# Optimization experiments

Hardware: AMD Instinct MI355X
Metric: run time of the kernel (lower is better)

## Reference

```python
import jax, jax.numpy as jnp
import numpy as np
from jax import lax

EPS_LN = 1e-5
EPS_BN = 1e-5

def layernorm(x, g, b):
    m = x.mean(-1, keepdims=True)
    v = x.var(-1, keepdims=True)
    return (x - m) / jnp.sqrt(v + EPS_LN) * g + b

def conv(x, w, b):
    y = lax.conv_general_dilated(x, w, (1, 1), 'SAME', dimension_numbers=('NCHW', 'OIHW', 'NCHW'))
    return y + b[None, :, None, None]

def bnorm(x, g, b, m, v):
    # BatchNorm2d in eval mode (running stats)
    return (x - m[None, :, None, None]) / jnp.sqrt(v[None, :, None, None] + EPS_BN) * g[None, :, None, None] + b[None, :, None, None]

def maxpool2(x):
    return lax.reduce_window(x, -jnp.inf, lax.max, (1, 1, 2, 2), (1, 1, 2, 2), 'VALID')

def l2norm_rows(x):
    n = jnp.linalg.norm(x, axis=1, keepdims=True)
    return x / jnp.maximum(n, 1e-12)

def fastslow(x, sw, sb, fw, fb, lng, lnb, lr, decay):
    # one hebbian fast-weight update step (torch does this in no_grad on x.detach())
    xs = lax.stop_gradient(x)
    fw = fw * decay
    fb = fb * decay
    slow_out = xs @ sw.T + sb
    xn = l2norm_rows(xs)
    son = l2norm_rows(slow_out)
    hebb = son.T @ xn / xs.shape[0]          # [out,in] outer-product update
    fw = fw + lr * hebb
    wn = jnp.linalg.norm(fw, axis=1, keepdims=True)
    fw = jnp.where(wn > 0.25, fw * (0.25 / (wn + 1e-8)), fw)
    fb = jnp.clip(fb + lr * son.mean(0), -0.2, 0.2)
    fw = lax.stop_gradient(fw)
    fb = lax.stop_gradient(fb)
    out = x @ (sw + fw).T + (sb + fb)
    return layernorm(out, lng, lnb)

def forward(x, c1_w, c1_b, bn1_g, bn1_b, bn1_m, bn1_v,
            c2_w, c2_b, bn2_g, bn2_b, bn2_m, bn2_v,
            c3_w, c3_b, bn3_g, bn3_b, bn3_m, bn3_v,
            core_w, core_b, core_lng, core_lnb,
            fp_sw, fp_sb, fp_fw, fp_fb, fp_lng, fp_lnb,
            sp_sw, sp_sb, sp_fw, sp_fb, sp_lng, sp_lnb,
            int_w, int_b, int_lng, int_lnb, mem,
            cn_w1, cn_b1, cn_lng, cn_lnb, cn_w2, cn_b2,
            pr_w, pr_b, pr_lng, pr_lnb, cl_w, cl_b):
    # encoder (dropout layers are identity in eval)
    h = jax.nn.relu(bnorm(conv(x, c1_w, c1_b), bn1_g, bn1_b, bn1_m, bn1_v)); h = maxpool2(h)
    h = jax.nn.relu(bnorm(conv(h, c2_w, c2_b), bn2_g, bn2_b, bn2_m, bn2_v)); h = maxpool2(h)
    h = jax.nn.relu(bnorm(conv(h, c3_w, c3_b), bn3_g, bn3_b, bn3_m, bn3_v))
    h = h.mean((2, 3))  # AdaptiveAvgPool2d((1,1)) + Flatten -> [B,256]
    # core
    hc = jax.nn.relu(layernorm(h @ core_w.T + core_b, core_lng, core_lnb))
    # dual system: memory EMA (no_grad), fast/slow hebbian paths, integrator
    mem_new = lax.stop_gradient(0.9 * mem + 0.1 * hc.mean(0, keepdims=True))
    fast_out = fastslow(hc, fp_sw, fp_sb, fp_fw, fp_fb, fp_lng, fp_lnb, 0.015, 0.95)
    slow_out = fastslow(hc + 0.3 * mem_new, sp_sw, sp_sb, sp_fw, sp_fb, sp_lng, sp_lnb, 0.005, 0.97)
    comb = jnp.concatenate([fast_out, slow_out], axis=1)
    hd = layernorm(comb @ int_w.T + int_b, int_lng, int_lnb)
    hd = hd + hc  # residual
    # consciousness: phi from eigen-entropy of feature covariance (no_grad)
    a = lax.stop_gradient(hd)
    am = a.mean(0, keepdims=True)
    ast = jnp.std(a, axis=0, keepdims=True, ddof=1) + 1e-6
    an = (a - am) / ast
    n = a.shape[0]
    cov = an.T @ an / (n - 1) + 1e-4 * jnp.eye(a.shape[1], dtype=a.dtype)
    eigs = jnp.clip(jnp.linalg.eigvalsh(cov), 0.0, None)
    en = eigs / (eigs.sum() + 1e-8)
    entropy = -(en * jnp.log(en + 1e-8)).sum()
    phi = entropy / jnp.log(jnp.asarray(float(a.shape[1]), a.dtype))
    phi_eff = jnp.clip(0.3 * phi, 0.0, 1.0)  # running_phi starts at 0: 0.7*0 + 0.3*phi
    net = jax.nn.relu(layernorm(hd @ cn_w1.T + cn_b1, cn_lng, cn_lnb)) @ cn_w2.T + cn_b2
    strength = jax.nn.sigmoid((phi_eff - 0.1) * 5.0)
    coef = jnp.where(phi_eff > 0.1, strength, 0.1)
    hcon = hd + coef * net
    # projection + classifier
    hp = jax.nn.relu(layernorm(hcon @ pr_w.T + pr_b, pr_lng, pr_lnb))
    return hp @ cl_w.T + cl_b

def setup_inputs() -> dict:
    key = jax.random.key(0)
    ks = iter(jax.random.split(key, 64))
    def nrm(shape, s=0.05):
        return jax.random.normal(next(ks), shape, jnp.float32) * s
    B, D = 512, 256
    d = {}
    d['x'] = jax.random.normal(next(ks), (B, 3, 32, 32), jnp.float32)
    for i, (co, ci) in enumerate([(64, 3), (128, 64), (256, 128)], 1):
        d[f'c{i}_w'] = nrm((co, ci, 3, 3))
        d[f'c{i}_b'] = jnp.zeros((co,), jnp.float32)
        d[f'bn{i}_g'] = jnp.ones((co,), jnp.float32)
        d[f'bn{i}_b'] = jnp.zeros((co,), jnp.float32)
        d[f'bn{i}_m'] = jnp.zeros((co,), jnp.float32)
        d[f'bn{i}_v'] = jnp.ones((co,), jnp.float32)
    d['core_w'] = nrm((D, D)); d['core_b'] = jnp.zeros((D,), jnp.float32)
    d['core_lng'] = jnp.ones((D,), jnp.float32); d['core_lnb'] = jnp.zeros((D,), jnp.float32)
    for p in ['fp', 'sp']:
        d[f'{p}_sw'] = nrm((D, D)); d[f'{p}_sb'] = jnp.zeros((D,), jnp.float32)
        d[f'{p}_fw'] = nrm((D, D), 0.01); d[f'{p}_fb'] = jnp.zeros((D,), jnp.float32)
        d[f'{p}_lng'] = jnp.ones((D,), jnp.float32); d[f'{p}_lnb'] = jnp.zeros((D,), jnp.float32)
    d['int_w'] = nrm((D, 2 * D)); d['int_b'] = jnp.zeros((D,), jnp.float32)
    d['int_lng'] = jnp.ones((D,), jnp.float32); d['int_lnb'] = jnp.zeros((D,), jnp.float32)
    d['mem'] = jnp.zeros((1, D), jnp.float32)
    d['cn_w1'] = nrm((D, D)); d['cn_b1'] = jnp.zeros((D,), jnp.float32)
    d['cn_lng'] = jnp.ones((D,), jnp.float32); d['cn_lnb'] = jnp.zeros((D,), jnp.float32)
    d['cn_w2'] = nrm((D, D)); d['cn_b2'] = jnp.zeros((D,), jnp.float32)
    d['pr_w'] = nrm((128, D)); d['pr_b'] = jnp.zeros((128,), jnp.float32)
    d['pr_lng'] = jnp.ones((128,), jnp.float32); d['pr_lnb'] = jnp.zeros((128,), jnp.float32)
    d['cl_w'] = nrm((10, 128)); d['cl_b'] = jnp.zeros((10,), jnp.float32)
    return d

def reference(x, c1_w, c1_b, bn1_g, bn1_b, bn1_m, bn1_v,
              c2_w, c2_b, bn2_g, bn2_b, bn2_m, bn2_v,
              c3_w, c3_b, bn3_g, bn3_b, bn3_m, bn3_v,
              core_w, core_b, core_lng, core_lnb,
              fp_sw, fp_sb, fp_fw, fp_fb, fp_lng, fp_lnb,
              sp_sw, sp_sb, sp_fw, sp_fb, sp_lng, sp_lnb,
              int_w, int_b, int_lng, int_lnb, mem,
              cn_w1, cn_b1, cn_lng, cn_lnb, cn_w2, cn_b2,
              pr_w, pr_b, pr_lng, pr_lnb, cl_w, cl_b):
    return forward(x, c1_w, c1_b, bn1_g, bn1_b, bn1_m, bn1_v,
                   c2_w, c2_b, bn2_g, bn2_b, bn2_m, bn2_v,
                   c3_w, c3_b, bn3_g, bn3_b, bn3_m, bn3_v,
                   core_w, core_b, core_lng, core_lnb,
                   fp_sw, fp_sb, fp_fw, fp_fb, fp_lng, fp_lnb,
                   sp_sw, sp_sb, sp_fw, sp_fb, sp_lng, sp_lnb,
                   int_w, int_b, int_lng, int_lnb, mem,
                   cn_w1, cn_b1, cn_lng, cn_lnb, cn_w2, cn_b2,
                   pr_w, pr_b, pr_lng, pr_lnb, cl_w, cl_b)
```

## Files before the change

### kernel.cpp

```cpp
#include <hip/hip_runtime.h>
#include <hip/hip_bf16.h>

template<int NT>
__device__ __forceinline__ float block_sum(float v, float* red, int t) {
  red[t] = v; __syncthreads();
#pragma unroll
  for (int s = NT/2; s > 0; s >>= 1) {
    if (t < s) red[t] += red[t+s];
    __syncthreads();
  }
  float r = red[0];
  __syncthreads();
  return r;
}

__device__ __forceinline__ float block_sum4(float val, float* red4, int t) {
#pragma unroll
  for (int mk = 1; mk < 64; mk <<= 1) val += __shfl_xor(val, mk, 64);
  if ((t & 63) == 0) red4[t >> 6] = val;
  __syncthreads();
  float r = red4[0] + red4[1] + red4[2] + red4[3];
  __syncthreads();
  return r;
}

template<int DIN>
__device__ __forceinline__ float dot_f32_row(const float* __restrict__ wr, const float* __restrict__ xs) {
  float acc = 0.f;
  const float4* wp = reinterpret_cast<const float4*>(wr);
#pragma unroll 4
  for (int i = 0; i < DIN/4; ++i) {
    float4 w4 = wp[i];
    acc += w4.x*xs[i*4] + w4.y*xs[i*4+1] + w4.z*xs[i*4+2] + w4.w*xs[i*4+3];
  }
  return acc;
}

__global__ __launch_bounds__(256) void k_conv1(const float* __restrict__ x, const float* __restrict__ w1,
    const float* __restrict__ cb, const float* __restrict__ g, const float* __restrict__ bb,
    const float* __restrict__ m, const float* __restrict__ v, float* __restrict__ p1)
{
  __shared__ float xs[3][34][34];
  __shared__ float ws1[64*27];
  __shared__ float A1[64], B1[64];
  int b = blockIdx.x, t = threadIdx.x;
  float* xsf = &xs[0][0][0];
  for (int i = t; i < 3*34*34; i += 256) xsf[i] = 0.f;
  for (int i = t; i < 64*27; i += 256) ws1[i] = w1[i];
  if (t < 64) {
    float sc = g[t] * rsqrtf(v[t] + 1e-5f);
    A1[t] = sc;
    B1[t] = (cb[t] - m[t])*sc + bb[t];
  }
  __syncthreads();
  for (int i = t; i < 3*1024; i += 256) {
    int ci = i >> 10, rem = i & 1023, y = rem >> 5, xx = rem & 31;
    xs[ci][y+1][xx+1] = x[((size_t)b*3 + ci)*1024 + rem];
  }
  __syncthreads();
  int py = t >> 4, px = t & 15;
  int y0 = py*2, x0 = px*2;
  for (int co = 0; co < 64; ++co) {
    float a00=0.f,a01=0.f,a10=0.f,a11=0.f;
#pragma unroll
    for (int ci = 0; ci < 3; ++ci) {
      const float* xb = &xs[ci][y0][x0];
      float r0a=xb[0],r0b=xb[1],r0c=xb[2],r0d=xb[3];
      float r1a=xb[34],r1b=xb[35],r1c=xb[36],r1d=xb[37];
      float r2a=xb[68],r2b=xb[69],r2c=xb[70],r2d=xb[71];
      float r3a=xb[102],r3b=xb[103],r3c=xb[104],r3d=xb[105];
      const float* wp = &ws1[co*27 + ci*9];
      float ww0=wp[0],ww1=wp[1],ww2=wp[2],ww3=wp[3],ww4=wp[4],ww5=wp[5],ww6=wp[6],ww7=wp[7],ww8=wp[8];
      a00 += ww0*r0a+ww1*r0b+ww2*r0c + ww3*r1a+ww4*r1b+ww5*r1c + ww6*r2a+ww7*r2b+ww8*r2c;
      a01 += ww0*r0b+ww1*r0c+ww2*r0d + ww3*r1b+ww4*r1c+ww5*r1d + ww6*r2b+ww7*r2c+ww8*r2d;
      a10 += ww0*r1a+ww1*r1b+ww2*r1c + ww3*r2a+ww4*r2b+ww5*r2c + ww6*r3a+ww7*r3b+ww8*r3c;
      a11 += ww0*r1b+ww1*r1c+ww2*r1d + ww3*r2b+ww4*r2c+ww5*r2d + ww6*r3b+ww7*r3c+ww8*r3d;
    }
    float sc = A1[co], sh = B1[co];
    float vmax = fmaxf(fmaxf(a00*sc+sh, a01*sc+sh), fmaxf(a10*sc+sh, a11*sc+sh));
    vmax = fmaxf(vmax, 0.f);
    p1[(((size_t)b*64 + co)*16 + py)*16 + px] = vmax;
  }
}

__global__ __launch_bounds__(256) void k_conv2(const float* __restrict__ p1, const float* __restrict__ w2,
    const float* __restrict__ cb, const float* __restrict__ g, const float* __restrict__ bb,
    const float* __restrict__ m, const float* __restrict__ v, float* __restrict__ p2)
{
  __shared__ float xs[64][18][18];
  __shared__ float wchT[576*5];
  __shared__ float A2[128], B2[128];
  int b = blockIdx.x, t = threadIdx.x;
  float* xsf = &xs[0][0][0];
  for (int i = t; i < 64*18*18; i += 256) xsf[i] = 0.f;
  if (t < 128) {
    float sc = g[t] * rsqrtf(v[t] + 1e-5f);
    A2[t] = sc;
    B2[t] = (cb[t] - m[t])*sc + bb[t];
  }
  __syncthreads();
  for (int i = t; i < 64*256; i += 256) {
    int ci = i >> 8, rem = i & 255, y = rem >> 4, xx = rem & 15;
    xs[ci][y+1][xx+1] = p1[((size_t)b*64 + ci)*256 + rem];
  }
  int lane = t & 3, pos = t >> 2;
  int py = pos >> 3, px = pos & 7;
  int y0 = py*2, x0 = px*2;
  for (int it = 0; it < 32; ++it) {
    __syncthreads();
    for (int i = t; i < 2304; i += 256) {
      int rem = i % 576, co = i / 576;
      wchT[rem*5 + co] = w2[(size_t)it*2304 + i];
    }
    __syncthreads();
    float a00=0.f,a01=0.f,a10=0.f,a11=0.f;
    for (int ci = 0; ci < 64; ++ci) {
      const float* xb = &xs[ci][y0][x0];
      float r0a=xb[0],r0b=xb[1],r0c=xb[2],r0d=xb[3];
      float r1a=xb[18],r1b=xb[19],r1c=xb[20],r1d=xb[21];
      float r2a=xb[36],r2b=xb[37],r2c=xb[38],r2d=xb[39];
      float r3a=xb[54],r3b=xb[55],r3c=xb[56],r3d=xb[57];
      const float* wp = &wchT[(ci*9)*5 + lane];
      float ww0=wp[0],ww1=wp[5],ww2=wp[10],ww3=wp[15],ww4=wp[20],ww5=wp[25],ww6=wp[30],ww7=wp[35],ww8=wp[40];
      a00 += ww0*r0a+ww1*r0b+ww2*r0c + ww3*r1a+ww4*r1b+ww5*r1c + ww6*r2a+ww7*r2b+ww8*r2c;
      a01 += ww0*r0b+ww1*r0c+ww2*r0d + ww3*r1b+ww4*r1c+ww5*r1d + ww6*r2b+ww7*r2c+ww8*r2d;
      a10 += ww0*r1a+ww1*r1b+ww2*r1c + ww3*r2a+ww4*r2b+ww5*r2c + ww6*r3a+ww7*r3b+ww8*r3c;
      a11 += ww0*r1b+ww1*r1c+ww2*r1d + ww3*r2b+ww4*r2c+ww5*r2d + ww6*r3b+ww7*r3c+ww8*r3d;
    }
    int co = it*4 + lane;
    float sc = A2[co], sh = B2[co];
    float vmax = fmaxf(fmaxf(a00*sc+sh, a01*sc+sh), fmaxf(a10*sc+sh, a11*sc+sh));
    vmax = fmaxf(vmax, 0.f);
    p2[(((size_t)b*128 + co)*8 + py)*8 + px] = vmax;
  }
}

__global__ __launch_bounds__(256) void k_conv3(const float* __restrict__ p2, const float* __restrict__ w3,
    const float* __restrict__ cb, const float* __restrict__ g, const float* __restrict__ bb,
    const float* __restrict__ m, const float* __restrict__ v, float* __restrict__ h)
{
  __shared__ float xs[128][10][10];
  __shared__ float wchT[1152*17];
  __shared__ float A3[256], B3[256];
  __shared__ float red2[256];
  int b = blockIdx.x, t = threadIdx.x;
  float* xsf = &xs[0][0][0];
  for (int i = t; i < 128*100; i += 256) xsf[i] = 0.f;
  {
    float sc = g[t] * rsqrtf(v[t] + 1e-5f);
    A3[t] = sc;
    B3[t] = (cb[t] - m[t])*sc + bb[t];
  }
  __syncthreads();
  for (int i = t; i < 128*64; i += 256) {
    int ci = i >> 6, rem = i & 63, y = rem >> 3, xx = rem & 7;
    xs[ci][y+1][xx+1] = p2[((size_t)b*128 + ci)*64 + rem];
  }
  int lane = t & 15, cluster = t >> 4;
  int cy = cluster >> 2, cx = cluster & 3;
  int y0 = cy*2, x0 = cx*2;
  for (int it = 0; it < 16; ++it) {
    __syncthreads();
    for (int i = t; i < 18432; i += 256) {
      int rem = i % 1152, co = i / 1152;
      wchT[rem*17 + co] = w3[(size_t)it*18432 + i];
    }
    __syncthreads();
    float a00=0.f,a01=0.f,a10=0.f,a11=0.f;
    for (int ci = 0; ci < 128; ++ci) {
      const float* xb = &xs[ci][y0][x0];
      float r0a=xb[0],r0b=xb[1],r0c=xb[2],r0d=xb[3];
      float r1a=xb[10],r1b=xb[11],r1c=xb[12],r1d=xb[13];
      float r2a=xb[20],r2b=xb[21],r2c=xb[22],r2d=xb[23];
      float r3a=xb[30],r3b=xb[31],r3c=xb[32],r3d=xb[33];
      const float* wp = &wchT[(ci*9)*17 + lane];
      float ww0=wp[0],ww1=wp[17],ww2=wp[34],ww3=wp[51],ww4=wp[68],ww5=wp[85],ww6=wp[102],ww7=wp[119],ww8=wp[136];
      a00 += ww0*r0a+ww1*r0b+ww2*r0c + ww3*r1a+ww4*r1b+ww5*r1c + ww6*r2a+ww7*r2b+ww8*r2c;
      a01 += ww0*r0b+ww1*r0c+ww2*r0d + ww3*r1b+ww4*r1c+ww5*r1d + ww6*r2b+ww7*r2c+ww8*r2d;
      a10 += ww0*r1a+ww1*r1b+ww2*r1c + ww3*r2a+ww4*r2b+ww5*r2c + ww6*r3a+ww7*r3b+ww8*r3c;
      a11 += ww0*r1b+ww1*r1c+ww2*r1d + ww3*r2b+ww4*r2c+ww5*r2d + ww6*r3b+ww7*r3c+ww8*r3d;
    }
    int co = it*16 + lane;
    float sc = A3[co], sh = B3[co];
    float local = fmaxf(a00*sc+sh,0.f)+fmaxf(a01*sc+sh,0.f)+fmaxf(a10*sc+sh,0.f)+fmaxf(a11*sc+sh,0.f);
    red2[cluster*16 + lane] = local;
    __syncthreads();
    if (t < 16) {
      float s2 = 0.f;
      for (int c2 = 0; c2 < 16; ++c2) s2 += red2[c2*16 + t];
      h[(size_t)b*256 + it*16 + t] = s2 * (1.f/64.f);
    }
  }
}

template<int DIN, int DOUT, bool RELU, bool RESID>
__global__ __launch_bounds__(DOUT) void k_lin_ln(
    const float* __restrict__ in, const float* __restrict__ W, const float* __restrict__ bias,
    const float* __restrict__ g, const float* __restrict__ be,
    const float* __restrict__ resid, float* __restrict__ out, int ostride, int ooff)
{
  __shared__ float xs[DIN];
  __shared__ float red[DOUT];
  int b = blockIdx.x, t = threadIdx.x;
  for (int i = t; i < DIN; i += DOUT) xs[i] = in[(size_t)b*DIN + i];
  __syncthreads();
  float acc = dot_f32_row<DIN>(W + (size_t)t*DIN, xs) + bias[t];
  float mean = block_sum<DOUT>(acc, red, t) * (1.f/DOUT);
  float dv = acc - mean;
  float var = block_sum<DOUT>(dv*dv, red, t) * (1.f/DOUT);
  float y = dv * rsqrtf(var + 1e-5f) * g[t] + be[t];
  if (RELU) y = fmaxf(y, 0.f);
  if (RESID) y += resid[(size_t)b*DOUT + t];
  out[(size_t)b*ostride + ooff + t] = y;
}

__global__ __launch_bounds__(256) void k_lin_rownorm(const float* __restrict__ in, const float* __restrict__ sw,
    const float* __restrict__ sb, float* __restrict__ sout, float* __restrict__ xninv, float* __restrict__ sninv)
{
  int b = blockIdx.x, t = threadIdx.x;
  __shared__ float xs[256];
  __shared__ float red[256];
  xs[t] = in[(size_t)b*256 + t];
  __syncthreads();
  float acc = dot_f32_row<256>(sw + (size_t)t*256, xs) + sb[t];
  sout[(size_t)b*256 + t] = acc;
  float xn2 = block_sum<256>(xs[t]*xs[t], red, t);
  float sn2 = block_sum<256>(acc*acc, red, t);
  if (t == 0) {
    xninv[b] = 1.f / fmaxf(sqrtf(xn2), 1e-12f);
    sninv[b] = 1.f / fmaxf(sqrtf(sn2), 1e-12f);
  }
}

__global__ __launch_bounds__(256) void k_hebb(const float* __restrict__ x, const float* __restrict__ s,
    const float* __restrict__ xninv, const float* __restrict__ sninv,
    const float* __restrict__ sw, const float* __restrict__ fw,
    const float* __restrict__ sb, const float* __restrict__ fb,
    float lr, float decay, float* __restrict__ weff, float* __restrict__ beff)
{
  int o = blockIdx.x, t = threadIdx.x;
  __shared__ float c[512];
  __shared__ float sonb[512];
  __shared__ float red[256];
  for (int b = t; b < 512; b += 256) {
    float son = s[(size_t)b*256 + o] * sninv[b];
    sonb[b] = son;
    c[b] = son * xninv[b];
  }
  __syncthreads();
  float acc = 0.f;
  for (int b = 0; b < 512; ++b) acc += c[b] * x[(size_t)b*256 + t];
  float hebb = acc * (1.f/512.f);
  float fwn = fw[(size_t)o*256 + t] * decay + lr * hebb;
  float wn2 = block_sum<256>(fwn*fwn, red, t);
  float wn = sqrtf(wn2);
  float scale = (wn > 0.25f) ? 0.25f/(wn + 1e-8f) : 1.f;
  weff[(size_t)o*256 + t] = sw[(size_t)o*256 + t] + fwn*scale;
  float sm = block_sum<256>(sonb[t] + sonb[t+256], red, t) * (1.f/512.f);
  if (t == 0) {
    float fbe = fb[o] * decay + lr * sm;
    fbe = fminf(fmaxf(fbe, -0.2f), 0.2f);
    beff[o] = sb[o] + fbe;
  }
}

__global__ __launch_bounds__(256) void k_mem(const float* __restrict__ hc, const float* __restrict__ mem,
                                             float* __restrict__ memnew)
{
  int t = threadIdx.x;
  float s = 0.f;
  for (int b = 0; b < 512; ++b) s += hc[(size_t)b*256 + t];
  memnew[t] = 0.9f*mem[t] + 0.1f*(s * (1.f/512.f));
}

__global__ __launch_bounds__(256) void k_x2(const float* __restrict__ hc, const float* __restrict__ memnew,
                                            float* __restrict__ x2)
{
  int i = blockIdx.x*256 + threadIdx.x;
  x2[i] = hc[i] + 0.3f*memnew[i & 255];
}

__global__ __launch_bounds__(256) void k_colstats(const float* __restrict__ hd, float* __restrict__ am,
                                                  float* __restrict__ ainv)
{
  int t = threadIdx.x;
  float s1 = 0.f;
  for (int b = 0; b < 512; ++b) s1 += hd[(size_t)b*256 + t];
  float mean = s1 * (1.f/512.f);
  float s2 = 0.f;
  for (int b = 0; b < 512; ++b) { float dv = hd[(size_t)b*256 + t] - mean; s2 += dv*dv; }
  am[t] = mean;
  ainv[t] = 1.f/(sqrtf(s2 * (1.f/511.f)) + 1e-6f);
}

__global__ __launch_bounds__(256) void k_cov(const float* __restrict__ hd, const float* __restrict__ am,
    const float* __restrict__ ainv, float* __restrict__ cov)
{
  int i = blockIdx.x, t = threadIdx.x;
  __shared__ float ci[512];
  float ami = am[i], aii = ainv[i];
  for (int b = t; b < 512; b += 256) ci[b] = (hd[(size_t)b*256 + i] - ami)*aii;
  __syncthreads();
  float amj = am[t], aij = ainv[t];
  float acc = 0.f;
  for (int b = 0; b < 512; ++b) acc += ci[b] * (hd[(size_t)b*256 + t] - amj);
  float cval = acc * aij * (1.f/511.f) + ((i == t) ? 1e-4f : 0.f);
  cov[(size_t)i*256 + t] = cval;
}

__global__ __launch_bounds__(256) void k_tridiag(const float* __restrict__ A, float* __restrict__ d, float* __restrict__ e)
{
  const int n = 256;
  __shared__ float tri[32896];
  __shared__ float v[256], q[256];
  __shared__ float red4[4];
  __shared__ float sH, salpha;
  int t = threadIdx.x;

  for (int i = t; i < 32896; i += 256) {
    int r = (int)((sqrtf(8.f*(float)i + 1.f) - 1.f) * 0.5f);
    while ((r+1)*(r+2)/2 <= i) ++r;
    while (r*(r+1)/2 > i) --r;
    int c = i - r*(r+1)/2;
    tri[i] = A[(size_t)r*n + c];
  }
  __syncthreads();

  for (int k = 0; k < n-2; ++k) {
    int m = n-1-k;
    int base = k+1;
    int R = base + t;
    int offA = (R*(R+1))/2 + base;
    float xi = (t < m) ? tri[offA - 1] : 0.f;
    float sigma = block_sum4(xi*xi, red4, t);
    if (t == 0) {
      float x0 = tri[(base*(base+1))/2 + k];
      float alpha = (x0 >= 0.f) ? -sqrtf(sigma) : sqrtf(sigma);
      salpha = alpha;
      sH = sigma - x0*alpha;
      e[k] = alpha;
    }
    __syncthreads();
    float H = sH;
    if (H <= 1e-32f) { __syncthreads(); continue; }
    if (t < m) v[t] = (t == 0) ? (xi - salpha) : xi;
    __syncthreads();

    float pt = 0.f;
    if (t < m) {
      float a0 = 0.f, a1 = 0.f, a2 = 0.f, a3 = 0.f;
      int j = 0;
      for (; j + 4 <= t+1; j += 4) {
        a0 += tri[offA + j]     * v[j];
        a1 += tri[offA + j + 1] * v[j+1];
        a2 += tri[offA + j + 2] * v[j+2];
        a3 += tri[offA + j + 3] * v[j+3];
      }
      for (; j <= t; ++j) a0 += tri[offA + j] * v[j];
      int Rj = R + 1;
      int off = (Rj*(Rj+1))/2 + R;
      for (j = t+1; j + 4 <= m; j += 4) {
        int o0 = off;
        int o1 = o0 + (base + j + 1);
        int o2 = o1 + (base + j + 2);
        int o3 = o2 + (base + j + 3);
        a0 += tri[o0] * v[j];
        a1 += tri[o1] * v[j+1];
        a2 += tri[o2] * v[j+2];
        a3 += tri[o3] * v[j+3];
        off = o3 + (base + j + 4);
      }
      for (; j < m; ++j) {
        a0 += tri[off] * v[j];
        off += (base + j + 1);
      }
      pt = (a0 + a1 + a2 + a3) / H;
    }
    float Kv = block_sum4((t < m) ? v[t]*pt : 0.f, red4, t) / (2.f*H);
    if (t < m) q[t] = pt - Kv*v[t];
    __syncthreads();

    if (t < m) {
      float vt = v[t], qt = q[t];
      int c = 0;
      for (; c + 4 <= t+1; c += 4) {
        float u0 = tri[offA + c]     - (vt*q[c]   + qt*v[c]);
        float u1 = tri[offA + c + 1] - (vt*q[c+1] + qt*v[c+1]);
        float u2 = tri[offA + c + 2] - (vt*q[c+2] + qt*v[c+2]);
        float u3 = tri[offA + c + 3] - (vt*q[c+3] + qt*v[c+3]);
        tri[offA + c]     = u0;
        tri[offA + c + 1] = u1;
        tri[offA + c + 2] = u2;
        tri[offA + c + 3] = u3;
      }
      for (; c <= t; ++c) tri[offA + c] -= vt*q[c] + qt*v[c];
    }
    __syncthreads();
  }
  if (t == 0) {
    e[n-2] = tri[((n-1)*n)/2 + (n-2)];
    e[n-1] = 0.f;
  }
  d[t] = tri[(t*(t+1))/2 + t];
}

__global__ __launch_bounds__(256) void k_eig_coef(const float* __restrict__ dg, const float* __restrict__ eg,
                                                  float* __restrict__ coefout)
{
  const int n = 256;
  int t = threadIdx.x;
  __shared__ float sd[256], se2[256], sea[256], red[256];
  sd[t] = dg[t];
  float ev = (t < n-1) ? eg[t] : 0.f;
  se2[t] = ev*ev;
  sea[t] = fabsf(ev);
  __syncthreads();
  float r = ((t > 0) ? sea[t-1] : 0.f) + sea[t];
  red[t] = sd[t] - r; __syncthreads();
  for (int s = 128; s > 0; s >>= 1) { if (t < s) red[t] = fminf(red[t], red[t+s]); __syncthreads(); }
  float glo = red[0] - 1e-3f; __syncthreads();
  red[t] = sd[t] + r; __syncthreads();
  for (int s = 128; s > 0; s >>= 1) { if (t < s) red[t] = fmaxf(red[t], red[t+s]); __syncthreads(); }
  float ghi = red[0] + 1e-3f; __syncthreads();

  float lo = glo, hi = ghi;
  for (int it = 0; it < 40; ++it) {
    float mid = 0.5f*(lo + hi);
    int cnt = 0;
    float qq = sd[0] - mid;
    cnt += (qq < 0.f);
    for (int i = 1; i < n; ++i) {
      float denom = qq;
      if (fabsf(denom) < 1e-20f) denom = (denom < 0.f) ? -1e-20f : 1e-20f;
      qq = sd[i] - mid - se2[i-1]/denom;
      cnt += (qq < 0.f);
    }
    if (cnt <= t) lo = mid; else hi = mid;
  }
  float lam = fmaxf(0.5f*(lo + hi), 0.f);
  float tot = block_sum<256>(lam, red, t) + 1e-8f;
  float en = lam / tot;
  float contrib = -en * logf(en + 1e-8f);
  float ent = block_sum<256>(contrib, red, t);
  if (t == 0) {
    float phi = ent / logf(256.f);
    float phi_eff = fminf(fmaxf(0.3f*phi, 0.f), 1.f);
    float strength = 1.f/(1.f + expf(-(phi_eff - 0.1f)*5.f));
    coefout[0] = (phi_eff > 0.1f) ? strength : 0.1f;
  }
}

__global__ __launch_bounds__(256) void k_cn2(const float* __restrict__ t1, const float* __restrict__ W,
    const float* __restrict__ bias, const float* __restrict__ hd, const float* __restrict__ coefp,
    float* __restrict__ hcon)
{
  __shared__ float xs[256];
  int b = blockIdx.x, t = threadIdx.x;
  xs[t] = t1[(size_t)b*256 + t];
  __syncthreads();
  float acc = dot_f32_row<256>(W + (size_t)t*256, xs) + bias[t];
  hcon[(size_t)b*256 + t] = hd[(size_t)b*256 + t] + coefp[0]*acc;
}

__global__ __launch_bounds__(64) void k_cls(const float* __restrict__ hp, const float* __restrict__ W,
    const float* __restrict__ bias, float* __restrict__ out)
{
  int b = blockIdx.x, t = threadIdx.x;
  __shared__ float xs[128];
  if (t < 64) { xs[t] = hp[(size_t)b*128 + t]; xs[t+64] = hp[(size_t)b*128 + t + 64]; }
  __syncthreads();
  if (t < 10) {
    float acc = bias[t];
    const float* wr = W + (size_t)t*128;
    for (int i = 0; i < 128; ++i) acc += wr[i]*xs[i];
    out[(size_t)b*10 + t] = acc;
  }
}

extern "C" void kernel_launch(void* const* d_in, const int* in_sizes, int n_in,
                              void* d_out, int out_size, void* d_ws, size_t ws_size,
                              hipStream_t stream)
{
  (void)in_sizes; (void)n_in; (void)out_size; (void)ws_size;
  const float* x     = (const float*)d_in[0];
  const float* c1w   = (const float*)d_in[1];
  const float* c1b   = (const float*)d_in[2];
  const float* bn1g  = (const float*)d_in[3];
  const float* bn1b  = (const float*)d_in[4];
  const float* bn1m  = (const float*)d_in[5];
  const float* bn1v  = (const float*)d_in[6];
  const float* c2w   = (const float*)d_in[7];
  const float* c2b   = (const float*)d_in[8];
  const float* bn2g  = (const float*)d_in[9];
  const float* bn2b  = (const float*)d_in[10];
  const float* bn2m  = (const float*)d_in[11];
  const float* bn2v  = (const float*)d_in[12];
  const float* c3w   = (const float*)d_in[13];
  const float* c3b   = (const float*)d_in[14];
  const float* bn3g  = (const float*)d_in[15];
  const float* bn3b  = (const float*)d_in[16];
  const float* bn3m  = (const float*)d_in[17];
  const float* bn3v  = (const float*)d_in[18];
  const float* corew = (const float*)d_in[19];
  const float* coreb = (const float*)d_in[20];
  const float* corelng = (const float*)d_in[21];
  const float* corelnb = (const float*)d_in[22];
  const float* fpsw  = (const float*)d_in[23];
  const float* fpsb  = (const float*)d_in[24];
  const float* fpfw  = (const float*)d_in[25];
  const float* fpfb  = (const float*)d_in[26];
  const float* fplng = (const float*)d_in[27];
  const float* fplnb = (const float*)d_in[28];
  const float* spsw  = (const float*)d_in[29];
  const float* spsb  = (const float*)d_in[30];
  const float* spfw  = (const float*)d_in[31];
  const float* spfb  = (const float*)d_in[32];
  const float* splng = (const float*)d_in[33];
  const float* splnb = (const float*)d_in[34];
  const float* intw  = (const float*)d_in[35];
  const float* intb  = (const float*)d_in[36];
  const float* intlng= (const float*)d_in[37];
  const float* intlnb= (const float*)d_in[38];
  const float* memi  = (const float*)d_in[39];
  const float* cnw1  = (const float*)d_in[40];
  const float* cnb1  = (const float*)d_in[41];
  const float* cnlng = (const float*)d_in[42];
  const float* cnlnb = (const float*)d_in[43];
  const float* cnw2  = (const float*)d_in[44];
  const float* cnb2  = (const float*)d_in[45];
  const float* prw   = (const float*)d_in[46];
  const float* prb   = (const float*)d_in[47];
  const float* prlng = (const float*)d_in[48];
  const float* prlnb = (const float*)d_in[49];
  const float* clw   = (const float*)d_in[50];
  const float* clb   = (const float*)d_in[51];
  float* out = (float*)d_out;

  float* w = (float*)d_ws;
  size_t off = 0;
  auto alloc = [&](size_t nel) { float* p = w + off; off += nel; return p; };
  float* p1     = alloc((size_t)512*64*16*16);
  float* p2     = alloc((size_t)512*128*8*8);
  float* h      = alloc(512*256);
  float* hc     = alloc(512*256);
  float* x2     = alloc(512*256);
  float* s      = alloc(512*256);
  float* xninv  = alloc(512);
  float* sninv  = alloc(512);
  float* memnew = alloc(256);
  float* weff   = alloc(256*256);
  float* beff   = alloc(256);
  float* comb   = alloc((size_t)512*512);
  float* hd     = alloc(512*256);
  float* am     = alloc(256);
  float* ainv   = alloc(256);
  float* cov    = alloc(256*256);
  float* dvec   = alloc(256);
  float* evec   = alloc(256);
  float* coefb  = alloc(8);
  float* t1     = alloc(512*256);
  float* hcon   = alloc(512*256);
  float* hp     = alloc(512*128);

  k_conv1<<<512,256,0,stream>>>(x, c1w, c1b, bn1g, bn1b, bn1m, bn1v, p1);
  k_conv2<<<512,256,0,stream>>>(p1, c2w, c2b, bn2g, bn2b, bn2m, bn2v, p2);
  k_conv3<<<512,256,0,stream>>>(p2, c3w, c3b, bn3g, bn3b, bn3m, bn3v, h);
  k_lin_ln<256,256,true,false><<<512,256,0,stream>>>(h, corew, coreb, corelng, corelnb, nullptr, hc, 256, 0);
  k_mem<<<1,256,0,stream>>>(hc, memi, memnew);
  k_x2<<<512,256,0,stream>>>(hc, memnew, x2);
  k_lin_rownorm<<<512,256,0,stream>>>(hc, fpsw, fpsb, s, xninv, sninv);
  k_hebb<<<256,256,0,stream>>>(hc, s, xninv, sninv, fpsw, fpfw, fpsb, fpfb, 0.015f, 0.95f, weff, beff);
  k_lin_ln<256,256,false,false><<<512,256,0,stream>>>(hc, weff, beff, fplng, fplnb, nullptr, comb, 512, 0);
  k_lin_rownorm<<<512,256,0,stream>>>(x2, spsw, spsb, s, xninv, sninv);
  k_hebb<<<256,256,0,stream>>>(x2, s, xninv, sninv, spsw, spfw, spsb, spfb, 0.005f, 0.97f, weff, beff);
  k_lin_ln<256,256,false,false><<<512,256,0,stream>>>(x2, weff, beff, splng, splnb, nullptr, comb, 512, 256);
  k_lin_ln<512,256,false,true><<<512,256,0,stream>>>(comb, intw, intb, intlng, intlnb, hc, hd, 256, 0);
  k_colstats<<<1,256,0,stream>>>(hd, am, ainv);
  k_cov<<<256,256,0,stream>>>(hd, am, ainv, cov);
  k_tridiag<<<1,256,0,stream>>>(cov, dvec, evec);
  k_eig_coef<<<1,256,0,stream>>>(dvec, evec, coefb);
  k_lin_ln<256,256,true,false><<<512,256,0,stream>>>(hd, cnw1, cnb1, cnlng, cnlnb, nullptr, t1, 256, 0);
  k_cn2<<<512,256,0,stream>>>(t1, cnw2, cnb2, hd, coefb, hcon);
  k_lin_ln<256,128,true,false><<<512,128,0,stream>>>(hcon, prw, prb, prlng, prlnb, nullptr, hp, 128, 0);
  k_cls<<<512,64,0,stream>>>(hp, clw, clb, out);
}
```

Baseline: 4.820 ms.

## Split each tridiagonalization row across four threads in a 1024-thread block

The single-block Householder tridiagonalization now runs with 1024 threads, giving four threads per matrix row. Each thread takes a quarter of the matrix-vector product and of the rank-2 update, with partial sums combined through shared memory, and the row-contiguous parts use aligned float4 LDS accesses. The aim is to shorten the long serial per-step work on the critical path of this one-block kernel. In exchange it adds a shared-memory partial-sum pass and a 16-wave reduction, and the per-step barriers now synchronise many more waves.

```diff
diff --git a/kernel.cpp b/kernel.cpp
--- a/kernel.cpp
+++ b/kernel.cpp
@@ -10,16 +10,6 @@
     __syncthreads();
   }
   float r = red[0];
-  __syncthreads();
-  return r;
-}
-
-__device__ __forceinline__ float block_sum4(float val, float* red4, int t) {
-#pragma unroll
-  for (int mk = 1; mk < 64; mk <<= 1) val += __shfl_xor(val, mk, 64);
-  if ((t & 63) == 0) red4[t >> 6] = val;
-  __syncthreads();
-  float r = red4[0] + red4[1] + red4[2] + red4[3];
   __syncthreads();
   return r;
 }
@@ -308,16 +298,18 @@
   cov[(size_t)i*256 + t] = cval;
 }
 
-__global__ __launch_bounds__(256) void k_tridiag(const float* __restrict__ A, float* __restrict__ d, float* __restrict__ e)
+__global__ __launch_bounds__(1024) void k_tridiag(const float* __restrict__ A, float* __restrict__ d, float* __restrict__ e)
 {
   const int n = 256;
   __shared__ float tri[32896];
   __shared__ float v[256], q[256];
-  __shared__ float red4[4];
+  __shared__ float pp[1024];
+  __shared__ float red16[16];
   __shared__ float sH, salpha;
   int t = threadIdx.x;
-
-  for (int i = t; i < 32896; i += 256) {
+  int r4 = t >> 2, s = t & 3;
+
+  for (int i = t; i < 32896; i += 1024) {
     int r = (int)((sqrtf(8.f*(float)i + 1.f) - 1.f) * 0.5f);
     while ((r+1)*(r+2)/2 <= i) ++r;
     while (r*(r+1)/2 > i) --r;
@@ -329,71 +321,100 @@
   for (int k = 0; k < n-2; ++k) {
     int m = n-1-k;
     int base = k+1;
-    int R = base + t;
+    int R = base + r4;
     int offA = (R*(R+1))/2 + base;
-    float xi = (t < m) ? tri[offA - 1] : 0.f;
-    float sigma = block_sum4(xi*xi, red4, t);
+    bool act = (r4 < m);
+
+    float xi = 0.f;
+    if (act && s == 0) {
+      xi = tri[offA - 1];
+      v[r4] = xi;
+    }
+    float val = xi*xi;
+#pragma unroll
+    for (int mk2 = 1; mk2 < 64; mk2 <<= 1) val += __shfl_xor(val, mk2, 64);
+    if ((t & 63) == 0) red16[t >> 6] = val;
+    __syncthreads();
     if (t == 0) {
-      float x0 = tri[(base*(base+1))/2 + k];
+      float sigma = 0.f;
+#pragma unroll
+      for (int i2 = 0; i2 < 16; ++i2) sigma += red16[i2];
+      float x0 = v[0];
       float alpha = (x0 >= 0.f) ? -sqrtf(sigma) : sqrtf(sigma);
       salpha = alpha;
       sH = sigma - x0*alpha;
       e[k] = alpha;
+      v[0] = x0 - alpha;
     }
     __syncthreads();
     float H = sH;
-    if (H <= 1e-32f) { __syncthreads(); continue; }
-    if (t < m) v[t] = (t == 0) ? (xi - salpha) : xi;
-    __syncthreads();
-
-    float pt = 0.f;
-    if (t < m) {
-      float a0 = 0.f, a1 = 0.f, a2 = 0.f, a3 = 0.f;
-      int j = 0;
-      for (; j + 4 <= t+1; j += 4) {
-        a0 += tri[offA + j]     * v[j];
-        a1 += tri[offA + j + 1] * v[j+1];
-        a2 += tri[offA + j + 2] * v[j+2];
-        a3 += tri[offA + j + 3] * v[j+3];
+    if (H <= 1e-32f) continue;
+
+    int j0 = (s * m) >> 2;
+    int j1 = ((s + 1) * m) >> 2;
+    float acc = 0.f;
+    if (act) {
+      int jr_end = min(j1, r4 + 1);
+      int j = j0;
+      for (; j < jr_end && ((offA + j) & 3); ++j) acc += tri[offA + j] * v[j];
+      for (; j + 4 <= jr_end; j += 4) {
+        float4 a4 = *reinterpret_cast<const float4*>(&tri[offA + j]);
+        acc += a4.x*v[j] + a4.y*v[j+1] + a4.z*v[j+2] + a4.w*v[j+3];
       }
-      for (; j <= t; ++j) a0 += tri[offA + j] * v[j];
-      int Rj = R + 1;
-      int off = (Rj*(Rj+1))/2 + R;
-      for (j = t+1; j + 4 <= m; j += 4) {
-        int o0 = off;
-        int o1 = o0 + (base + j + 1);
-        int o2 = o1 + (base + j + 2);
-        int o3 = o2 + (base + j + 3);
-        a0 += tri[o0] * v[j];
-        a1 += tri[o1] * v[j+1];
-        a2 += tri[o2] * v[j+2];
-        a3 += tri[o3] * v[j+3];
-        off = o3 + (base + j + 4);
+      for (; j < jr_end; ++j) acc += tri[offA + j] * v[j];
+      j = max(j0, r4 + 1);
+      if (j < j1) {
+        int Rj = base + j;
+        int off = (Rj*(Rj+1))/2 + R;
+        for (; j + 4 <= j1; j += 4) {
+          int o0 = off;
+          int o1 = o0 + (base + j + 1);
+          int o2 = o1 + (base + j + 2);
+          int o3 = o2 + (base + j + 3);
+          acc += tri[o0]*v[j] + tri[o1]*v[j+1] + tri[o2]*v[j+2] + tri[o3]*v[j+3];
+          off = o3 + (base + j + 4);
+        }
+        for (; j < j1; ++j) { acc += tri[off]*v[j]; off += base + j + 1; }
       }
-      for (; j < m; ++j) {
-        a0 += tri[off] * v[j];
-        off += (base + j + 1);
+    }
+    pp[t] = acc;
+    __syncthreads();
+
+    float kvpart = 0.f;
+    float p_r = 0.f;
+    if (act && s == 0) {
+      p_r = (pp[4*r4] + pp[4*r4+1] + pp[4*r4+2] + pp[4*r4+3]) / H;
+      kvpart = v[r4] * p_r;
+    }
+#pragma unroll
+    for (int mk2 = 1; mk2 < 64; mk2 <<= 1) kvpart += __shfl_xor(kvpart, mk2, 64);
+    if ((t & 63) == 0) red16[t >> 6] = kvpart;
+    __syncthreads();
+    if (act && s == 0) {
+      float Kv = 0.f;
+#pragma unroll
+      for (int i2 = 0; i2 < 16; ++i2) Kv += red16[i2];
+      Kv /= (2.f*H);
+      q[r4] = p_r - Kv*v[r4];
+    }
+    __syncthreads();
+
+    if (act) {
+      int len = r4 + 1;
+      int c0 = (s*len) >> 2;
+      int c1 = ((s+1)*len) >> 2;
+      float vt = v[r4], qt = q[r4];
+      int c = c0;
+      for (; c < c1 && ((offA + c) & 3); ++c) tri[offA + c] -= vt*q[c] + qt*v[c];
+      for (; c + 4 <= c1; c += 4) {
+        float4 a4 = *reinterpret_cast<const float4*>(&tri[offA + c]);
+        a4.x -= vt*q[c]   + qt*v[c];
+        a4.y -= vt*q[c+1] + qt*v[c+1];
+        a4.z -= vt*q[c+2] + qt*v[c+2];
+        a4.w -= vt*q[c+3] + qt*v[c+3];
+        *reinterpret_cast<float4*>(&tri[offA + c]) = a4;
       }
-      pt = (a0 + a1 + a2 + a3) / H;
-    }
-    float Kv = block_sum4((t < m) ? v[t]*pt : 0.f, red4, t) / (2.f*H);
-    if (t < m) q[t] = pt - Kv*v[t];
-    __syncthreads();
-
-    if (t < m) {
-      float vt = v[t], qt = q[t];
-      int c = 0;
-      for (; c + 4 <= t+1; c += 4) {
-        float u0 = tri[offA + c]     - (vt*q[c]   + qt*v[c]);
-        float u1 = tri[offA + c + 1] - (vt*q[c+1] + qt*v[c+1]);
-        float u2 = tri[offA + c + 2] - (vt*q[c+2] + qt*v[c+2]);
-        float u3 = tri[offA + c + 3] - (vt*q[c+3] + qt*v[c+3]);
-        tri[offA + c]     = u0;
-        tri[offA + c + 1] = u1;
-        tri[offA + c + 2] = u2;
-        tri[offA + c + 3] = u3;
-      }
-      for (; c <= t; ++c) tri[offA + c] -= vt*q[c] + qt*v[c];
+      for (; c < c1; ++c) tri[offA + c] -= vt*q[c] + qt*v[c];
     }
     __syncthreads();
   }
@@ -401,7 +422,7 @@
     e[n-2] = tri[((n-1)*n)/2 + (n-2)];
     e[n-1] = 0.f;
   }
-  d[t] = tri[(t*(t+1))/2 + t];
+  if (t < n) d[t] = tri[(t*(t+1))/2 + t];
 }
 
 __global__ __launch_bounds__(256) void k_eig_coef(const float* __restrict__ dg, const float* __restrict__ eg,
@@ -577,7 +598,7 @@
   k_lin_ln<512,256,false,true><<<512,256,0,stream>>>(comb, intw, intb, intlng, intlnb, hc, hd, 256, 0);
   k_colstats<<<1,256,0,stream>>>(hd, am, ainv);
   k_cov<<<256,256,0,stream>>>(hd, am, ainv, cov);
-  k_tridiag<<<1,256,0,stream>>>(cov, dvec, evec);
+  k_tridiag<<<1,1024,0,stream>>>(cov, dvec, evec);
   k_eig_coef<<<1,256,0,stream>>>(dvec, evec, coefb);
   k_lin_ln<256,256,true,false><<<512,256,0,stream>>>(hd, cnw1, cnb1, cnlng, cnlnb, nullptr, t1, 256, 0);
   k_cn2<<<512,256,0,stream>>>(t1, cnw2, cnb2, hd, coefb, hcon);
```

After: 4.740 ms. No clear change (-1.7%).

## Parallelize Householder tridiagonalization across 1024 threads with wave-per-row symmetric matvec

Applied to the files above, without the earlier changes.

The single-block tridiagonal reduction now launches 1024 threads instead of 256 and assigns each packed lower-triangle row to a wavefront. Each wave computes both the row dot product and the transposed contributions in one pass, accumulating per-wave partials in shared memory that are then summed. The old scheme had one thread per row walking strided column entries serially, which was load-imbalanced and latency-bound on this serial critical-path kernel. The new scheme adds an extra partial-sum buffer and more barriers per step, and occupancy stays one block.

```diff
diff --git a/kernel.cpp b/kernel.cpp
--- a/kernel.cpp
+++ b/kernel.cpp
@@ -10,16 +10,6 @@
     __syncthreads();
   }
   float r = red[0];
-  __syncthreads();
-  return r;
-}
-
-__device__ __forceinline__ float block_sum4(float val, float* red4, int t) {
-#pragma unroll
-  for (int mk = 1; mk < 64; mk <<= 1) val += __shfl_xor(val, mk, 64);
-  if ((t & 63) == 0) red4[t >> 6] = val;
-  __syncthreads();
-  float r = red4[0] + red4[1] + red4[2] + red4[3];
   __syncthreads();
   return r;
 }
@@ -308,16 +298,18 @@
   cov[(size_t)i*256 + t] = cval;
 }
 
-__global__ __launch_bounds__(256) void k_tridiag(const float* __restrict__ A, float* __restrict__ d, float* __restrict__ e)
+__global__ __launch_bounds__(1024) void k_tridiag(const float* __restrict__ A, float* __restrict__ d, float* __restrict__ e)
 {
   const int n = 256;
   __shared__ float tri[32896];
   __shared__ float v[256], q[256];
-  __shared__ float red4[4];
-  __shared__ float sH, salpha;
+  __shared__ float ppw[16][257];
+  __shared__ float redA[4], red4[4];
+  __shared__ float sH;
   int t = threadIdx.x;
-
-  for (int i = t; i < 32896; i += 256) {
+  int wid = t >> 6, lane = t & 63;
+
+  for (int i = t; i < 32896; i += 1024) {
     int r = (int)((sqrtf(8.f*(float)i + 1.f) - 1.f) * 0.5f);
     while ((r+1)*(r+2)/2 <= i) ++r;
     while (r*(r+1)/2 > i) --r;
@@ -329,71 +321,93 @@
   for (int k = 0; k < n-2; ++k) {
     int m = n-1-k;
     int base = k+1;
-    int R = base + t;
-    int offA = (R*(R+1))/2 + base;
-    float xi = (t < m) ? tri[offA - 1] : 0.f;
-    float sigma = block_sum4(xi*xi, red4, t);
+
+    float xi = 0.f;
+    if (t < m) {
+      int R = base + t;
+      xi = tri[R*(R+1)/2 + k];
+      v[t] = xi;
+    }
+    if (t < 256) {
+      float val = xi*xi;
+#pragma unroll
+      for (int mk = 1; mk < 64; mk <<= 1) val += __shfl_xor(val, mk, 64);
+      if (lane == 0) redA[wid] = val;
+    }
+    __syncthreads();
     if (t == 0) {
-      float x0 = tri[(base*(base+1))/2 + k];
+      float sigma = redA[0]+redA[1]+redA[2]+redA[3];
+      float x0 = v[0];
       float alpha = (x0 >= 0.f) ? -sqrtf(sigma) : sqrtf(sigma);
-      salpha = alpha;
       sH = sigma - x0*alpha;
       e[k] = alpha;
+      v[0] = x0 - alpha;
     }
     __syncthreads();
     float H = sH;
-    if (H <= 1e-32f) { __syncthreads(); continue; }
-    if (t < m) v[t] = (t == 0) ? (xi - salpha) : xi;
+    if (H <= 1e-32f) continue;
+
+    float p0=0.f, p1=0.f, p2=0.f, p3=0.f;
+    for (int r = wid; r < m; r += 16) {
+      int R = base + r;
+      int rowoff = R*(R+1)/2 + base;
+      float vr = v[r];
+      float dot = 0.f;
+#pragma unroll
+      for (int c = 0; c < 4; ++c) {
+        if (64*c <= r) {
+          int j = 64*c + lane;
+          float val = (j <= r) ? tri[rowoff + j] : 0.f;
+          dot += val * v[j];
+          float sval = (j < r) ? val : 0.f;
+          float contrib = sval * vr;
+          if (c == 0) p0 += contrib; else if (c == 1) p1 += contrib;
+          else if (c == 2) p2 += contrib; else p3 += contrib;
+        }
+      }
+#pragma unroll
+      for (int mk = 1; mk < 64; mk <<= 1) dot += __shfl_xor(dot, mk, 64);
+      if (lane == (r & 63)) {
+        int sl = r >> 6;
+        if (sl == 0) p0 += dot; else if (sl == 1) p1 += dot;
+        else if (sl == 2) p2 += dot; else p3 += dot;
+      }
+    }
+    ppw[wid][lane]      = p0;
+    ppw[wid][64+lane]   = p1;
+    ppw[wid][128+lane]  = p2;
+    ppw[wid][192+lane]  = p3;
     __syncthreads();
 
     float pt = 0.f;
+    if (t < 256) {
+      float kv = 0.f;
+#pragma unroll
+      for (int w2 = 0; w2 < 16; ++w2) pt += ppw[w2][t];
+      pt /= H;
+      if (t < m) kv = v[t] * pt;
+#pragma unroll
+      for (int mk = 1; mk < 64; mk <<= 1) kv += __shfl_xor(kv, mk, 64);
+      if (lane == 0) red4[wid] = kv;
+    }
+    __syncthreads();
     if (t < m) {
-      float a0 = 0.f, a1 = 0.f, a2 = 0.f, a3 = 0.f;
-      int j = 0;
-      for (; j + 4 <= t+1; j += 4) {
-        a0 += tri[offA + j]     * v[j];
-        a1 += tri[offA + j + 1] * v[j+1];
-        a2 += tri[offA + j + 2] * v[j+2];
-        a3 += tri[offA + j + 3] * v[j+3];
+      float Kv = (red4[0]+red4[1]+red4[2]+red4[3]) / (2.f*H);
+      q[t] = pt - Kv*v[t];
+    }
+    __syncthreads();
+
+    for (int r = wid; r < m; r += 16) {
+      int R = base + r;
+      int rowoff = R*(R+1)/2 + base;
+      float vr = v[r], qr = q[r];
+#pragma unroll
+      for (int c = 0; c < 4; ++c) {
+        if (64*c <= r) {
+          int j = 64*c + lane;
+          if (j <= r) tri[rowoff + j] -= vr*q[j] + qr*v[j];
+        }
       }
-      for (; j <= t; ++j) a0 += tri[offA + j] * v[j];
-      int Rj = R + 1;
-      int off = (Rj*(Rj+1))/2 + R;
-      for (j = t+1; j + 4 <= m; j += 4) {
-        int o0 = off;
-        int o1 = o0 + (base + j + 1);
-        int o2 = o1 + (base + j + 2);
-        int o3 = o2 + (base + j + 3);
-        a0 += tri[o0] * v[j];
-        a1 += tri[o1] * v[j+1];
-        a2 += tri[o2] * v[j+2];
-        a3 += tri[o3] * v[j+3];
-        off = o3 + (base + j + 4);
-      }
-      for (; j < m; ++j) {
-        a0 += tri[off] * v[j];
-        off += (base + j + 1);
-      }
-      pt = (a0 + a1 + a2 + a3) / H;
-    }
-    float Kv = block_sum4((t < m) ? v[t]*pt : 0.f, red4, t) / (2.f*H);
-    if (t < m) q[t] = pt - Kv*v[t];
-    __syncthreads();
-
-    if (t < m) {
-      float vt = v[t], qt = q[t];
-      int c = 0;
-      for (; c + 4 <= t+1; c += 4) {
-        float u0 = tri[offA + c]     - (vt*q[c]   + qt*v[c]);
-        float u1 = tri[offA + c + 1] - (vt*q[c+1] + qt*v[c+1]);
-        float u2 = tri[offA + c + 2] - (vt*q[c+2] + qt*v[c+2]);
-        float u3 = tri[offA + c + 3] - (vt*q[c+3] + qt*v[c+3]);
-        tri[offA + c]     = u0;
-        tri[offA + c + 1] = u1;
-        tri[offA + c + 2] = u2;
-        tri[offA + c + 3] = u3;
-      }
-      for (; c <= t; ++c) tri[offA + c] -= vt*q[c] + qt*v[c];
     }
     __syncthreads();
   }
@@ -401,7 +415,7 @@
     e[n-2] = tri[((n-1)*n)/2 + (n-2)];
     e[n-1] = 0.f;
   }
-  d[t] = tri[(t*(t+1))/2 + t];
+  if (t < n) d[t] = tri[(t*(t+1))/2 + t];
 }
 
 __global__ __launch_bounds__(256) void k_eig_coef(const float* __restrict__ dg, const float* __restrict__ eg,
@@ -577,7 +591,7 @@
   k_lin_ln<512,256,false,true><<<512,256,0,stream>>>(comb, intw, intb, intlng, intlnb, hc, hd, 256, 0);
   k_colstats<<<1,256,0,stream>>>(hd, am, ainv);
   k_cov<<<256,256,0,stream>>>(hd, am, ainv, cov);
-  k_tridiag<<<1,256,0,stream>>>(cov, dvec, evec);
+  k_tridiag<<<1,1024,0,stream>>>(cov, dvec, evec);
   k_eig_coef<<<1,256,0,stream>>>(dvec, evec, coefb);
   k_lin_ln<256,256,true,false><<<512,256,0,stream>>>(hd, cnw1, cnb1, cnlng, cnlnb, nullptr, t1, 256, 0);
   k_cn2<<<512,256,0,stream>>>(t1, cnw2, cnb2, hd, coefb, hcon);
```

After: 4.172 ms. -13.4%, faster.
